# Performance work log

Measured on AMD Instinct MI355X. Metric: run time of the kernel, lower is better.

Reference implementation:

```python
import jax, jax.numpy as jnp
import numpy as np

NEG_SLOPE = 0.2


def gat_conv(x, edge_src, edge_dst, W, att_src, att_dst, bias):
    """PyG-style GATConv (eval mode, concat=True, self-loops already appended).
    x: [N, F_in]; W: [F_in, H*C]; att_src/att_dst: [H, C]; bias: [H*C]."""
    N = x.shape[0]
    H, C = att_src.shape
    h = (x @ W).reshape(N, H, C)                      # [N,H,C]
    a_src = jnp.einsum('nhc,hc->nh', h, att_src)      # [N,H]
    a_dst = jnp.einsum('nhc,hc->nh', h, att_dst)      # [N,H]
    e = a_src[edge_src] + a_dst[edge_dst]             # [E',H]
    e = jax.nn.leaky_relu(e, NEG_SLOPE)
    # segment softmax over incoming edges per destination node
    e_max = jax.ops.segment_max(e, edge_dst, num_segments=N)   # [N,H]
    ex = jnp.exp(e - e_max[edge_dst])
    denom = jax.ops.segment_sum(ex, edge_dst, num_segments=N)  # [N,H]
    alpha = ex / denom[edge_dst]                       # [E',H]
    msg = h[edge_src] * alpha[:, :, None]              # [E',H,C]
    out = jax.ops.segment_sum(msg, edge_dst, num_segments=N)   # [N,H,C]
    return out.reshape(N, H * C) + bias


def setup_inputs() -> dict:
    key = jax.random.key(0)
    ks = jax.random.split(key, 16)
    N, E = 50000, 1600000
    x = jax.random.normal(ks[0], (N, 8), dtype=jnp.float32)
    edge_index = jax.random.randint(ks[1], (2, E), 0, N, dtype=jnp.int64)
    def glorot(k, shape):
        fan = sum(shape[-2:]) if len(shape) > 1 else shape[-1]
        return jax.random.normal(k, shape, dtype=jnp.float32) * (2.0 / fan) ** 0.5
    return {
        'x': x,
        'edge_index': edge_index,
        'W1': glorot(ks[2], (8, 32)),
        'att_src1': glorot(ks[3], (2, 16)),
        'att_dst1': glorot(ks[4], (2, 16)),
        'b1': jnp.zeros((32,), jnp.float32),
        'W2': glorot(ks[5], (32, 64)),
        'att_src2': glorot(ks[6], (2, 32)),
        'att_dst2': glorot(ks[7], (2, 32)),
        'b2': jnp.zeros((64,), jnp.float32),
        'fc1_w': glorot(ks[8], (64, 64)),
        'fc1_b': jnp.zeros((64,), jnp.float32),
        'fc2_w': glorot(ks[9], (64, 1)),
        'fc2_b': jnp.zeros((1,), jnp.float32),
    }


def reference(x, edge_index, W1, att_src1, att_dst1, b1, W2, att_src2, att_dst2, b2,
              fc1_w, fc1_b, fc2_w, fc2_b):
    N = x.shape[0]
    row, col = edge_index[0], edge_index[1]
    # GATConv adds self-loops internally (add_self_loops=True default)
    loops = jnp.arange(N, dtype=edge_index.dtype)
    src = jnp.concatenate([row, loops])
    dst = jnp.concatenate([col, loops])
    h = gat_conv(x, src, dst, W1, att_src1, att_dst1, b1)
    h = jax.nn.relu(h)
    h = gat_conv(h, src, dst, W2, att_src2, att_dst2, b2)
    h = jax.nn.relu(h)
    # edge-level head uses the ORIGINAL edge_index (no self-loops)
    e = h[row] + h[col]                                # [E,64]
    e = jax.nn.relu(e @ fc1_w + fc1_b)
    return e @ fc2_w + fc2_b                           # [E,1]
```

## Files before the change

kernel.cpp:

```cpp
#include <hip/hip_runtime.h>
#include <hip/hip_fp16.h>
#include <math.h>

#define NEG_SLOPE 0.2f
#define BKT_SHIFT 8
#define EPB 8192
#define MAXB 10240

__global__ void k_node1(const float* __restrict__ x, const float* __restrict__ W1,
                        const float* __restrict__ as1, const float* __restrict__ ad1,
                        __half* __restrict__ h1h, float* __restrict__ a_src1,
                        float* __restrict__ a_dst1, int N) {
    int n = blockIdx.x * blockDim.x + threadIdx.x;
    if (n >= N) return;
    float xv[8];
#pragma unroll
    for (int k = 0; k < 8; k++) xv[k] = x[n * 8 + k];
    float h[32];
#pragma unroll
    for (int j = 0; j < 32; j++) {
        float acc = 0.f;
#pragma unroll
        for (int k = 0; k < 8; k++) acc += xv[k] * W1[k * 32 + j];
        h[j] = acc;
        h1h[n * 32 + j] = __float2half(acc);
    }
#pragma unroll
    for (int hh = 0; hh < 2; hh++) {
        float s = 0.f, d = 0.f;
#pragma unroll
        for (int c = 0; c < 16; c++) {
            s += h[hh * 16 + c] * as1[hh * 16 + c];
            d += h[hh * 16 + c] * ad1[hh * 16 + c];
        }
        a_src1[n * 2 + hh] = s;
        a_dst1[n * 2 + hh] = d;
    }
}

__global__ __launch_bounds__(256) void k_bktA(const int* __restrict__ ei,
                                              int* __restrict__ bktCur,
                                              int2* __restrict__ bktbuf, int E, int K) {
    __shared__ int bh[256];
    __shared__ int bbase[256];
    __shared__ int loff[256];
    __shared__ int2 staged[EPB];
    __shared__ int gptr[EPB];
    int tid = threadIdx.x;
    int e0 = blockIdx.x * EPB;
    int e1 = e0 + EPB; if (e1 > E) e1 = E;
    int cnt = e1 - e0;
    bh[tid] = 0;
    __syncthreads();
    for (int i = e0 + tid; i < e1; i += 256)
        atomicAdd(&bh[ei[E + i] >> BKT_SHIFT], 1);
    __syncthreads();
    if (tid == 0) {
        int r = 0;
        for (int b = 0; b < K; b++) { loff[b] = r; r += bh[b]; }
    }
    if (tid < K) {
        int c = bh[tid];
        bbase[tid] = c > 0 ? atomicAdd(&bktCur[tid], c) : 0;
    }
    __syncthreads();
    bh[tid] = 0;
    __syncthreads();
    for (int i = e0 + tid; i < e1; i += 256) {
        int s = ei[i], d = ei[E + i];
        int b = d >> BKT_SHIFT, dl = d & 255;
        int r = atomicAdd(&bh[b], 1);
        int lp = loff[b] + r;
        staged[lp] = make_int2(s | (dl << 16), i);
        gptr[lp] = b * MAXB + bbase[b] + r;
    }
    __syncthreads();
    for (int i = tid; i < cnt; i += 256)
        bktbuf[gptr[i]] = staged[i];
}

__global__ void k_bktscan(const int* __restrict__ bktCur, int* __restrict__ bktOff, int K) {
    int lane = threadIdx.x;
    int chunk = (K + 63) >> 6;
    int beg = lane * chunk;
    int end = beg + chunk; if (end > K) end = K;
    int s = 0;
    for (int i = beg; i < end; i++) s += bktCur[i];
    int incl = s;
#pragma unroll
    for (int off = 1; off < 64; off <<= 1) {
        int v = __shfl_up(incl, off);
        if (lane >= off) incl += v;
    }
    int run = incl - s;
    for (int i = beg; i < end; i++) { bktOff[i] = run; run += bktCur[i]; }
    if (end == K) bktOff[K] = run;
}

__global__ __launch_bounds__(256) void k_bktB(const int* __restrict__ bktCur,
                                              const int* __restrict__ bktOff,
                                              const int2* __restrict__ bktbuf,
                                              int* __restrict__ rowp, int2* __restrict__ slotv,
                                              int N, int E, int K) {
    __shared__ int lhist[256];
    __shared__ int lrow[257];
    __shared__ int2 lslot[MAXB + 256];
    int k = blockIdx.x;
    int tid = threadIdx.x;
    int n0 = k << BKT_SHIFT;
    int nn = N - n0; if (nn > 256) nn = 256;
    int cnt = bktCur[k];
    int gbase = bktOff[k] + n0;
    lhist[tid] = 0;
    __syncthreads();
    const int2* rec = bktbuf + (size_t)k * MAXB;
    for (int i = tid; i < cnt; i += 256)
        atomicAdd(&lhist[(rec[i].x >> 16) & 255], 1);
    __syncthreads();
    if (tid == 0) {
        int r = 0;
        for (int i = 0; i < nn; i++) { lrow[i] = r; r += lhist[i] + 1; }
        lrow[nn] = r;
    }
    __syncthreads();
    if (tid < nn) {
        int lr = lrow[tid];
        rowp[n0 + tid] = gbase + lr;
        lslot[lr] = make_int2(n0 + tid, -1);
        lhist[tid] = lr + 1;
    }
    if (k == 0 && tid == 0) rowp[N] = E + N;
    __syncthreads();
    for (int i = tid; i < cnt; i += 256) {
        int2 rv = rec[i];
        int dl = (rv.x >> 16) & 255;
        int p = atomicAdd(&lhist[dl], 1);
        lslot[p] = make_int2(rv.x & 0xFFFF, rv.y);
    }
    __syncthreads();
    int tot = cnt + nn;
    for (int i = tid; i < tot; i += 256)
        slotv[gbase + i] = lslot[i];
}

__global__ void k_conv1(const int* __restrict__ rowp, const int2* __restrict__ slotv,
                        const float* __restrict__ a_src, const float* __restrict__ a_dst,
                        const __half* __restrict__ h1h, const float* __restrict__ b1,
                        const float* __restrict__ W2, const float* __restrict__ as2,
                        const float* __restrict__ ad2,
                        __half* __restrict__ h2h, float* __restrict__ a_src2,
                        float* __restrict__ a_dst2, int N) {
    int lane = threadIdx.x & 63;
    int n = __builtin_amdgcn_readfirstlane((int)((blockIdx.x * blockDim.x + threadIdx.x) >> 6));
    if (n >= N) return;
    int sub = lane & 31;
    int eslot = lane >> 5;
    int hh = sub >> 4;
    int beg = rowp[n], end = rowp[n + 1];
    float2 adv = *(const float2*)(a_dst + 2 * (size_t)n);
    float mA = -1e30f, mB = -1e30f;
    for (int i = beg + sub; i < end; i += 32) {
        int s = ((const int*)slotv)[2 * i];
        float2 as = *(const float2*)(a_src + 2 * (size_t)s);
        float tA = as.x + adv.x; tA = fmaxf(tA, NEG_SLOPE * tA);
        float tB = as.y + adv.y; tB = fmaxf(tB, NEG_SLOPE * tB);
        mA = fmaxf(mA, tA); mB = fmaxf(mB, tB);
    }
#pragma unroll
    for (int off = 16; off >= 1; off >>= 1) {
        mA = fmaxf(mA, __shfl_xor(mA, off));
        mB = fmaxf(mB, __shfl_xor(mB, off));
    }
    float m = hh ? mB : mA;
    float ad = hh ? adv.y : adv.x;
    float denom = 0.f, acc = 0.f;
#pragma unroll 4
    for (int j = beg; j < end; j += 2) {
        int2 sv0 = slotv[j];
        int2 sv1 = slotv[j + 1];
        int s0 = sv0.x & 0xFFFF, s1 = sv1.x & 0xFFFF;
        float2 a0 = *(const float2*)(a_src + 2 * (size_t)s0);
        float2 a1 = *(const float2*)(a_src + 2 * (size_t)s1);
        int s = eslot ? s1 : s0;
        float av = hh ? (eslot ? a1.y : a0.y) : (eslot ? a1.x : a0.x);
        float t = av + ad;
        t = fmaxf(t, NEG_SLOPE * t);
        float wgt = __expf(t - m);
        if (j + eslot >= end) wgt = 0.f;
        acc += wgt * __half2float(h1h[s * 32 + sub]);
        denom += wgt;
    }
    acc += __shfl_xor(acc, 32);
    denom += __shfl_xor(denom, 32);
    float ov = fmaxf(acc / denom + b1[sub], 0.f);
    float acc2 = 0.f;
#pragma unroll
    for (int k = 0; k < 32; k++) acc2 += __shfl(ov, k, 32) * W2[k * 64 + lane];
    h2h[(size_t)n * 64 + lane] = __float2half(acc2);
    float p = acc2 * as2[lane];
    float q = acc2 * ad2[lane];
#pragma unroll
    for (int off = 16; off >= 1; off >>= 1) {
        p += __shfl_xor(p, off);
        q += __shfl_xor(q, off);
    }
    if ((lane & 31) == 0) {
        a_src2[n * 2 + (lane >> 5)] = p;
        a_dst2[n * 2 + (lane >> 5)] = q;
    }
}

__global__ void k_conv2(const int* __restrict__ rowp, const int2* __restrict__ slotv,
                        const float* __restrict__ a_src, const float* __restrict__ a_dst,
                        const __half* __restrict__ h2h, const float* __restrict__ b2,
                        const float* __restrict__ fw1, const float* __restrict__ fb1,
                        __half* __restrict__ gh, int N) {
    int lane = threadIdx.x & 63;
    int n = __builtin_amdgcn_readfirstlane((int)((blockIdx.x * blockDim.x + threadIdx.x) >> 6));
    if (n >= N) return;
    int hh = lane >> 5;
    int beg = rowp[n], end = rowp[n + 1];
    float2 adv = *(const float2*)(a_dst + 2 * (size_t)n);
    float mA = -1e30f, mB = -1e30f;
    for (int i = beg + lane; i < end; i += 64) {
        int s = ((const int*)slotv)[2 * i];
        float2 as = *(const float2*)(a_src + 2 * (size_t)s);
        float tA = as.x + adv.x; tA = fmaxf(tA, NEG_SLOPE * tA);
        float tB = as.y + adv.y; tB = fmaxf(tB, NEG_SLOPE * tB);
        mA = fmaxf(mA, tA); mB = fmaxf(mB, tB);
    }
#pragma unroll
    for (int off = 32; off >= 1; off >>= 1) {
        mA = fmaxf(mA, __shfl_xor(mA, off));
        mB = fmaxf(mB, __shfl_xor(mB, off));
    }
    float m = hh ? mB : mA;
    float ad = hh ? adv.y : adv.x;
    float denom = 0.f, acc = 0.f;
#pragma unroll 4
    for (int j = beg; j < end; j++) {
        int s = slotv[j].x;
        float2 as = *(const float2*)(a_src + 2 * (size_t)s);
        float t = (hh ? as.y : as.x) + ad;
        t = fmaxf(t, NEG_SLOPE * t);
        float wgt = __expf(t - m);
        acc += wgt * __half2float(h2h[(size_t)s * 64 + lane]);
        denom += wgt;
    }
    float res = fmaxf(acc / denom + b2[lane], 0.f);
    float gv = 0.5f * fb1[lane];
#pragma unroll
    for (int k = 0; k < 64; k++) gv += __shfl(res, k) * fw1[k * 64 + lane];
    gh[(size_t)n * 64 + lane] = __float2half(gv);
}

__global__ void k_head4(const int* __restrict__ rowp, const int2* __restrict__ slotv,
                        const __half* __restrict__ gh,
                        const float* __restrict__ w2, const float* __restrict__ b2,
                        float* __restrict__ out, int M, int N) {
    int t = blockIdx.x * blockDim.x + threadIdx.x;
    if (t >= M) return;
    int2 sv = slotv[t];
    int id = sv.y;
    if (id < 0) return;
    int lo = 0, hi = N;
    while (hi - lo > 1) {
        int mid = (lo + hi) >> 1;
        if (rowp[mid] <= t) lo = mid; else hi = mid;
    }
    int n = lo;
    int r = sv.x;
    const uint4* gr = (const uint4*)(gh + (size_t)r * 64);
    const uint4* gc = (const uint4*)(gh + (size_t)n * 64);
    float o = b2[0];
#pragma unroll
    for (int q = 0; q < 8; q++) {
        uint4 ua = gr[q], ub = gc[q];
#pragma unroll
        for (int w = 0; w < 4; w++) {
            unsigned a32 = (&ua.x)[w], b32 = (&ub.x)[w];
            float2 fa = __half22float2(*(const __half2*)&a32);
            float2 fb = __half22float2(*(const __half2*)&b32);
            int j = q * 8 + w * 2;
            o += fmaxf(fa.x + fb.x, 0.f) * w2[j];
            o += fmaxf(fa.y + fb.y, 0.f) * w2[j + 1];
        }
    }
    out[id] = o;
}

extern "C" void kernel_launch(void* const* d_in, const int* in_sizes, int n_in,
                              void* d_out, int out_size, void* d_ws, size_t ws_size,
                              hipStream_t stream) {
    const float* x   = (const float*)d_in[0];
    const int*   ei  = (const int*)d_in[1];
    const float* W1  = (const float*)d_in[2];
    const float* as1 = (const float*)d_in[3];
    const float* ad1 = (const float*)d_in[4];
    const float* b1  = (const float*)d_in[5];
    const float* W2  = (const float*)d_in[6];
    const float* as2 = (const float*)d_in[7];
    const float* ad2 = (const float*)d_in[8];
    const float* b2  = (const float*)d_in[9];
    const float* fw1 = (const float*)d_in[10];
    const float* fb1 = (const float*)d_in[11];
    const float* fw2 = (const float*)d_in[12];
    const float* fb2 = (const float*)d_in[13];
    float* out = (float*)d_out;

    int N = in_sizes[0] / 8;
    int E = in_sizes[1] / 2;
    int M = E + N;
    int K = (N + 255) >> BKT_SHIFT;

    float* h1slot = (float*)d_ws;
    float* asr1 = h1slot + (size_t)N * 32;
    float* adt1 = asr1 + (size_t)N * 2;
    float* out1 = adt1 + (size_t)N * 2;
    float* h2slot = out1 + (size_t)N * 32;
    float* asr2 = h2slot + (size_t)N * 64;
    float* adt2 = asr2 + (size_t)N * 2;
    int*   rowp = (int*)(adt2 + (size_t)N * 2);
    int2*  slotv = (int2*)(rowp + ((N + 2) & ~1));
    int*   bktCur = (int*)(slotv + M);
    int*   bktOff = bktCur + 256;
    int2*  bktbuf = (int2*)out1;
    __half* h1h = (__half*)h1slot;
    __half* h2h = (__half*)h2slot;
    __half* gh  = (__half*)d_ws;

    int B = 256;
    k_node1<<<(N + B - 1) / B, B, 0, stream>>>(x, W1, as1, ad1, h1h, asr1, adt1, N);
    hipMemsetAsync(bktCur, 0, 256 * sizeof(int), stream);
    k_bktA<<<(E + EPB - 1) / EPB, 256, 0, stream>>>(ei, bktCur, bktbuf, E, K);
    k_bktscan<<<1, 64, 0, stream>>>(bktCur, bktOff, K);
    k_bktB<<<K, 256, 0, stream>>>(bktCur, bktOff, bktbuf, rowp, slotv, N, E, K);
    {
        long long thr = (long long)N * 64;
        k_conv1<<<(int)((thr + B - 1) / B), B, 0, stream>>>(rowp, slotv, asr1, adt1, h1h, b1,
                                                            W2, as2, ad2, h2h, asr2, adt2, N);
    }
    {
        long long thr = (long long)N * 64;
        k_conv2<<<(int)((thr + B - 1) / B), B, 0, stream>>>(rowp, slotv, asr2, adt2, h2h, b2,
                                                            fw1, fb1, gh, N);
    }
    k_head4<<<(M + B - 1) / B, B, 0, stream>>>(rowp, slotv, gh, fw2, fb2, out, M, N);
}
```

Baseline: 256.3 us.

## Precompute edge softmax weights per 64-edge chunk into LDS for aggregation

In both GAT aggregation kernels, each wave now computes source indices and exp weights for 64 edges in parallel, stages them in shared memory, and reduces the denominator with shuffles. The inner gather loop then reads indices and weights from LDS instead of each lane redundantly loading slotv and a_src and computing exp per edge. This removes serialized redundant scalar/broadcast loads and transcendental work, at the cost of shared-memory traffic and reliance on intra-wave ordering without explicit barriers. The max pass in conv1 is also widened to use all 64 lanes.

```diff
diff --git a/kernel.cpp b/kernel.cpp
--- a/kernel.cpp
+++ b/kernel.cpp
@@ -143,15 +143,20 @@
         slotv[gbase + i] = lslot[i];
 }
 
-__global__ void k_conv1(const int* __restrict__ rowp, const int2* __restrict__ slotv,
-                        const float* __restrict__ a_src, const float* __restrict__ a_dst,
-                        const __half* __restrict__ h1h, const float* __restrict__ b1,
-                        const float* __restrict__ W2, const float* __restrict__ as2,
-                        const float* __restrict__ ad2,
-                        __half* __restrict__ h2h, float* __restrict__ a_src2,
-                        float* __restrict__ a_dst2, int N) {
-    int lane = threadIdx.x & 63;
-    int n = __builtin_amdgcn_readfirstlane((int)((blockIdx.x * blockDim.x + threadIdx.x) >> 6));
+__global__ __launch_bounds__(256) void k_conv1(
+        const int* __restrict__ rowp, const int2* __restrict__ slotv,
+        const float* __restrict__ a_src, const float* __restrict__ a_dst,
+        const __half* __restrict__ h1h, const float* __restrict__ b1,
+        const float* __restrict__ W2, const float* __restrict__ as2,
+        const float* __restrict__ ad2,
+        __half* __restrict__ h2h, float* __restrict__ a_src2,
+        float* __restrict__ a_dst2, int N) {
+    __shared__ int   lsS[4][64];
+    __shared__ float lsW[4][2][64];
+    int tid = threadIdx.x;
+    int lane = tid & 63;
+    int wv = tid >> 6;
+    int n = __builtin_amdgcn_readfirstlane((int)((blockIdx.x * blockDim.x + tid) >> 6));
     if (n >= N) return;
     int sub = lane & 31;
     int eslot = lane >> 5;
@@ -159,39 +164,49 @@
     int beg = rowp[n], end = rowp[n + 1];
     float2 adv = *(const float2*)(a_dst + 2 * (size_t)n);
     float mA = -1e30f, mB = -1e30f;
-    for (int i = beg + sub; i < end; i += 32) {
-        int s = ((const int*)slotv)[2 * i];
+    for (int i = beg + lane; i < end; i += 64) {
+        int s = slotv[i].x;
         float2 as = *(const float2*)(a_src + 2 * (size_t)s);
         float tA = as.x + adv.x; tA = fmaxf(tA, NEG_SLOPE * tA);
         float tB = as.y + adv.y; tB = fmaxf(tB, NEG_SLOPE * tB);
         mA = fmaxf(mA, tA); mB = fmaxf(mB, tB);
     }
 #pragma unroll
-    for (int off = 16; off >= 1; off >>= 1) {
+    for (int off = 32; off >= 1; off >>= 1) {
         mA = fmaxf(mA, __shfl_xor(mA, off));
         mB = fmaxf(mB, __shfl_xor(mB, off));
     }
-    float m = hh ? mB : mA;
-    float ad = hh ? adv.y : adv.x;
     float denom = 0.f, acc = 0.f;
+    for (int j0 = beg; j0 < end; j0 += 64) {
+        int idx = j0 + lane;
+        bool valid = idx < end;
+        int s = valid ? slotv[idx].x : 0;
+        float2 as = valid ? *(const float2*)(a_src + 2 * (size_t)s)
+                          : make_float2(0.f, 0.f);
+        float tA = as.x + adv.x; tA = fmaxf(tA, NEG_SLOPE * tA);
+        float tB = as.y + adv.y; tB = fmaxf(tB, NEG_SLOPE * tB);
+        float wA = valid ? __expf(tA - mA) : 0.f;
+        float wB = valid ? __expf(tB - mB) : 0.f;
+        lsS[wv][lane] = s;
+        lsW[wv][0][lane] = wA;
+        lsW[wv][1][lane] = wB;
+        float rA = wA, rB = wB;
+#pragma unroll
+        for (int off = 32; off >= 1; off >>= 1) {
+            rA += __shfl_xor(rA, off);
+            rB += __shfl_xor(rB, off);
+        }
+        denom += hh ? rB : rA;
+        int cnt = end - j0; if (cnt > 64) cnt = 64;
 #pragma unroll 4
-    for (int j = beg; j < end; j += 2) {
-        int2 sv0 = slotv[j];
-        int2 sv1 = slotv[j + 1];
-        int s0 = sv0.x & 0xFFFF, s1 = sv1.x & 0xFFFF;
-        float2 a0 = *(const float2*)(a_src + 2 * (size_t)s0);
-        float2 a1 = *(const float2*)(a_src + 2 * (size_t)s1);
-        int s = eslot ? s1 : s0;
-        float av = hh ? (eslot ? a1.y : a0.y) : (eslot ? a1.x : a0.x);
-        float t = av + ad;
-        t = fmaxf(t, NEG_SLOPE * t);
-        float wgt = __expf(t - m);
-        if (j + eslot >= end) wgt = 0.f;
-        acc += wgt * __half2float(h1h[s * 32 + sub]);
-        denom += wgt;
+        for (int jj = 0; jj < cnt; jj += 2) {
+            int e = jj + eslot;
+            int sj = lsS[wv][e];
+            float wgt = lsW[wv][hh][e];
+            acc += wgt * __half2float(h1h[sj * 32 + sub]);
+        }
     }
     acc += __shfl_xor(acc, 32);
-    denom += __shfl_xor(denom, 32);
     float ov = fmaxf(acc / denom + b1[sub], 0.f);
     float acc2 = 0.f;
 #pragma unroll
@@ -210,20 +225,25 @@
     }
 }
 
-__global__ void k_conv2(const int* __restrict__ rowp, const int2* __restrict__ slotv,
-                        const float* __restrict__ a_src, const float* __restrict__ a_dst,
-                        const __half* __restrict__ h2h, const float* __restrict__ b2,
-                        const float* __restrict__ fw1, const float* __restrict__ fb1,
-                        __half* __restrict__ gh, int N) {
-    int lane = threadIdx.x & 63;
-    int n = __builtin_amdgcn_readfirstlane((int)((blockIdx.x * blockDim.x + threadIdx.x) >> 6));
+__global__ __launch_bounds__(256) void k_conv2(
+        const int* __restrict__ rowp, const int2* __restrict__ slotv,
+        const float* __restrict__ a_src, const float* __restrict__ a_dst,
+        const __half* __restrict__ h2h, const float* __restrict__ b2,
+        const float* __restrict__ fw1, const float* __restrict__ fb1,
+        __half* __restrict__ gh, int N) {
+    __shared__ int   lsS[4][64];
+    __shared__ float lsW[4][2][64];
+    int tid = threadIdx.x;
+    int lane = tid & 63;
+    int wv = tid >> 6;
+    int n = __builtin_amdgcn_readfirstlane((int)((blockIdx.x * blockDim.x + tid) >> 6));
     if (n >= N) return;
     int hh = lane >> 5;
     int beg = rowp[n], end = rowp[n + 1];
     float2 adv = *(const float2*)(a_dst + 2 * (size_t)n);
     float mA = -1e30f, mB = -1e30f;
     for (int i = beg + lane; i < end; i += 64) {
-        int s = ((const int*)slotv)[2 * i];
+        int s = slotv[i].x;
         float2 as = *(const float2*)(a_src + 2 * (size_t)s);
         float tA = as.x + adv.x; tA = fmaxf(tA, NEG_SLOPE * tA);
         float tB = as.y + adv.y; tB = fmaxf(tB, NEG_SLOPE * tB);
@@ -234,18 +254,34 @@
         mA = fmaxf(mA, __shfl_xor(mA, off));
         mB = fmaxf(mB, __shfl_xor(mB, off));
     }
-    float m = hh ? mB : mA;
-    float ad = hh ? adv.y : adv.x;
     float denom = 0.f, acc = 0.f;
-#pragma unroll 4
-    for (int j = beg; j < end; j++) {
-        int s = slotv[j].x;
-        float2 as = *(const float2*)(a_src + 2 * (size_t)s);
-        float t = (hh ? as.y : as.x) + ad;
-        t = fmaxf(t, NEG_SLOPE * t);
-        float wgt = __expf(t - m);
-        acc += wgt * __half2float(h2h[(size_t)s * 64 + lane]);
-        denom += wgt;
+    for (int j0 = beg; j0 < end; j0 += 64) {
+        int idx = j0 + lane;
+        bool valid = idx < end;
+        int s = valid ? slotv[idx].x : 0;
+        float2 as = valid ? *(const float2*)(a_src + 2 * (size_t)s)
+                          : make_float2(0.f, 0.f);
+        float tA = as.x + adv.x; tA = fmaxf(tA, NEG_SLOPE * tA);
+        float tB = as.y + adv.y; tB = fmaxf(tB, NEG_SLOPE * tB);
+        float wA = valid ? __expf(tA - mA) : 0.f;
+        float wB = valid ? __expf(tB - mB) : 0.f;
+        lsS[wv][lane] = s;
+        lsW[wv][0][lane] = wA;
+        lsW[wv][1][lane] = wB;
+        float rA = wA, rB = wB;
+#pragma unroll
+        for (int off = 32; off >= 1; off >>= 1) {
+            rA += __shfl_xor(rA, off);
+            rB += __shfl_xor(rB, off);
+        }
+        denom += hh ? rB : rA;
+        int cnt = end - j0; if (cnt > 64) cnt = 64;
+#pragma unroll 8
+        for (int jj = 0; jj < cnt; jj++) {
+            int sj = lsS[wv][jj];
+            float wgt = lsW[wv][hh][jj];
+            acc += wgt * __half2float(h2h[(size_t)sj * 64 + lane]);
+        }
     }
     float res = fmaxf(acc / denom + b2[lane], 0.f);
     float gv = 0.5f * fb1[lane];
```

Result: faster. 237.8 us (-7.2%).
